# Optimization experiments

Measured on AMD Instinct MI355X. Metric: run time of the kernel, lower is better.

The kernel has to match this reference:

```python
import jax, jax.numpy as jnp
import numpy as np

HIDDEN = 768
N_HEADS = 12
D_HEAD = 64
B, T = 4, 2048


def setup_inputs() -> dict:
    key = jax.random.key(0)
    ks = jax.random.split(key, 5)
    s = 0.02
    return {
        "x": jax.random.normal(ks[0], (B, T, HIDDEN), dtype=jnp.float32),
        "w_q": jax.random.normal(ks[1], (HIDDEN, HIDDEN), dtype=jnp.float32) * s,
        "w_k": jax.random.normal(ks[2], (HIDDEN, HIDDEN), dtype=jnp.float32) * s,
        "w_v": jax.random.normal(ks[3], (HIDDEN, HIDDEN), dtype=jnp.float32) * s,
        "w_o": jax.random.normal(ks[4], (HIDDEN, HIDDEN), dtype=jnp.float32) * s,
    }


def reference(x, w_q, w_k, w_v, w_o):
    # nn.Linear applies x @ W^T; weights here are [out, in] like torch.
    b, t, h = x.shape
    q = (x @ w_q.T).reshape(b, t, N_HEADS, D_HEAD)
    k = (x @ w_k.T).reshape(b, t, N_HEADS, D_HEAD)
    v = (x @ w_v.T).reshape(b, t, N_HEADS, D_HEAD)
    # scores: [b, heads, t, t]
    scores = jnp.einsum("bqhd,bkhd->bhqk", q, k) / jnp.sqrt(jnp.float32(D_HEAD))
    weights = jax.nn.softmax(scores, axis=-1)
    # dropout p=0.0 -> identity
    ctx = jnp.einsum("bhqk,bkhd->bqhd", weights, v).reshape(b, t, h)
    return ctx @ w_o.T
```

## Files before the change

kernel.cpp:

```cpp
#include <hip/hip_runtime.h>

#define HIDDEN 768
#define NH 12
#define DH 64
#define BB 4
#define TT 2048
#define MTOT (BB * TT)

typedef __bf16 bf16x8 __attribute__((ext_vector_type(8)));
typedef short s16x8 __attribute__((ext_vector_type(8)));
typedef float f32x4 __attribute__((ext_vector_type(4)));

__device__ __forceinline__ unsigned short f2b(float f) {
    unsigned u = __builtin_bit_cast(unsigned, f);
    u += 0x7fffu + ((u >> 16) & 1u);
    return (unsigned short)(u >> 16);
}

__device__ __forceinline__ unsigned pack_bf16(float a, float b) {
    return __builtin_amdgcn_perm(__builtin_bit_cast(unsigned, b),
                                 __builtin_bit_cast(unsigned, a), 0x07060302u);
}

typedef const __attribute__((address_space(1))) unsigned int* gas_ptr;
typedef __attribute__((address_space(3))) unsigned int* las_ptr;
__device__ __forceinline__ void gload16(const void* g, void* l) {
    __builtin_amdgcn_global_load_lds((gas_ptr)(uintptr_t)g, (las_ptr)(uintptr_t)l, 16, 0, 0);
}

__global__ __launch_bounds__(256) void cvt_all(const float* __restrict__ x,
                                               const float* __restrict__ wq,
                                               const float* __restrict__ wk,
                                               const float* __restrict__ wv,
                                               const float* __restrict__ wo,
                                               unsigned short* __restrict__ out) {
    const size_t NX8 = (size_t)MTOT * HIDDEN / 8;
    const size_t NW8 = (size_t)HIDDEN * HIDDEN / 8;
    size_t i = (size_t)blockIdx.x * 256 + threadIdx.x;
    const float* src;
    size_t off = i;
    float scale = 1.0f;
    if (i < NX8) { src = x; }
    else if (i < NX8 + NW8) { src = wq; off = i - NX8; scale = 0.18033688011112042f; }
    else if (i < NX8 + 2 * NW8) { src = wk; off = i - NX8 - NW8; }
    else if (i < NX8 + 3 * NW8) { src = wv; off = i - NX8 - 2 * NW8; }
    else { src = wo; off = i - NX8 - 3 * NW8; }
    const float4* p = (const float4*)src + off * 2;
    float4 a = p[0], b = p[1];
    union { uint4 u; unsigned short s[8]; } t;
    t.s[0] = f2b(a.x * scale); t.s[1] = f2b(a.y * scale);
    t.s[2] = f2b(a.z * scale); t.s[3] = f2b(a.w * scale);
    t.s[4] = f2b(b.x * scale); t.s[5] = f2b(b.y * scale);
    t.s[6] = f2b(b.z * scale); t.s[7] = f2b(b.w * scale);
    ((uint4*)out)[i] = t.u;
}

template <int MODE, int MROWS>
__device__ __forceinline__ void gemm_body(const unsigned short* __restrict__ A,
                                          const unsigned short* __restrict__ Bm,
                                          float* __restrict__ Cf,
                                          unsigned short* __restrict__ Cb,
                                          int mBase, int nBase, int N) {
    __shared__ __align__(16) unsigned short Al[MROWS][64];
    __shared__ __align__(16) unsigned short Bl[128][64];
    const int MT = MROWS / 32;
    const int tid = threadIdx.x;
    const int lane = tid & 63;
    const int wave = tid >> 6;
    const int quad = lane >> 4;
    const int l16 = lane & 15;
    const int mw = (wave >> 1) * (MROWS / 2);
    const int nw = (wave & 1) * 64;
    const int r8 = lane >> 3;
    const int swiz = ((lane & 7) ^ r8) * 8;
    const unsigned short* Asrc = A + (size_t)(mBase + wave * (MROWS / 4) + r8) * HIDDEN + swiz;
    const unsigned short* Bsrc = Bm + (size_t)(nBase + wave * 32 + r8) * HIDDEN + swiz;

    f32x4 acc[MT][4];
#pragma unroll
    for (int mt = 0; mt < MT; ++mt)
#pragma unroll
        for (int nt = 0; nt < 4; ++nt) acc[mt][nt] = (f32x4){0.f, 0.f, 0.f, 0.f};

    for (int kb = 0; kb < HIDDEN / 64; ++kb) {
        if (kb) __syncthreads();
#pragma unroll
        for (int i = 0; i < MROWS / 32; ++i)
            gload16(Asrc + (size_t)i * 8 * HIDDEN + kb * 64,
                    &Al[wave * (MROWS / 4) + i * 8][0]);
#pragma unroll
        for (int j = 0; j < 4; ++j)
            gload16(Bsrc + (size_t)j * 8 * HIDDEN + kb * 64, &Bl[wave * 32 + j * 8][0]);
        __syncthreads();
#pragma unroll
        for (int ks = 0; ks < 2; ++ks) {
            const int cc = ((ks * 4 + quad) ^ (l16 & 7)) * 8;
            bf16x8 af[MT], bf[4];
#pragma unroll
            for (int mt = 0; mt < MT; ++mt)
                af[mt] = *(const bf16x8*)&Al[mw + mt * 16 + l16][cc];
#pragma unroll
            for (int nt = 0; nt < 4; ++nt)
                bf[nt] = *(const bf16x8*)&Bl[nw + nt * 16 + l16][cc];
#pragma unroll
            for (int mt = 0; mt < MT; ++mt)
#pragma unroll
                for (int nt = 0; nt < 4; ++nt)
                    acc[mt][nt] = __builtin_amdgcn_mfma_f32_16x16x32_bf16(
                        af[mt], bf[nt], acc[mt][nt], 0, 0, 0);
        }
    }

#pragma unroll
    for (int mt = 0; mt < MT; ++mt)
#pragma unroll
        for (int nt = 0; nt < 4; ++nt) {
            if (MODE == 2) {
                ushort4 h;
                h.x = f2b(acc[mt][nt][0]); h.y = f2b(acc[mt][nt][1]);
                h.z = f2b(acc[mt][nt][2]); h.w = f2b(acc[mt][nt][3]);
                int m0 = mBase + mw + mt * 16 + quad * 4;
                int col = nBase + nw + nt * 16 + l16;
                *(ushort4*)&Cb[(size_t)col * MTOT + m0] = h;
            } else {
#pragma unroll
                for (int r = 0; r < 4; ++r) {
                    int row = mBase + mw + mt * 16 + quad * 4 + r;
                    int col = nBase + nw + nt * 16 + l16;
                    float v = acc[mt][nt][r];
                    if (MODE == 1)
                        Cf[(size_t)row * N + col] = v;
                    else
                        Cb[(size_t)row * N + col] = f2b(v);
                }
            }
        }
}

__global__ __launch_bounds__(256, 2) void gemm_qkv(const unsigned short* __restrict__ A,
                                                   const unsigned short* __restrict__ W0,
                                                   unsigned short* __restrict__ C0,
                                                   unsigned short* __restrict__ VT) {
    __shared__ __align__(16) unsigned short Al[64][64];
    __shared__ __align__(16) unsigned short Bl[3][128][64];
    const size_t NWW = (size_t)HIDDEN * HIDDEN;
    const size_t NX = (size_t)MTOT * HIDDEN;
    const int tid = threadIdx.x;
    const int lane = tid & 63;
    const int wave = tid >> 6;
    const int quad = lane >> 4;
    const int l16 = lane & 15;
    const int rx = l16 & 7;
    const int mw = (wave >> 1) * 32;
    const int nw = (wave & 1) * 64;
    const int r8 = lane >> 3;
    const int swiz = ((lane & 7) ^ r8) * 8;
    const int mBase = blockIdx.x * 64;
    const int nBase = blockIdx.y * 128;
    const unsigned short* Asrc = A + (size_t)(mBase + wave * 16 + r8) * HIDDEN + swiz;
    const unsigned short* Bsrc = W0 + (size_t)(nBase + wave * 32 + r8) * HIDDEN + swiz;

    f32x4 acc[3][2][4];
#pragma unroll
    for (int w = 0; w < 3; ++w)
#pragma unroll
        for (int mt = 0; mt < 2; ++mt)
#pragma unroll
            for (int nt = 0; nt < 4; ++nt) acc[w][mt][nt] = (f32x4){0.f, 0.f, 0.f, 0.f};

    for (int kb = 0; kb < HIDDEN / 64; ++kb) {
        if (kb) __syncthreads();
#pragma unroll
        for (int i = 0; i < 2; ++i)
            gload16(Asrc + (size_t)i * 8 * HIDDEN + kb * 64, &Al[wave * 16 + i * 8][0]);
#pragma unroll
        for (int w = 0; w < 3; ++w)
#pragma unroll
            for (int j = 0; j < 4; ++j)
                gload16(Bsrc + (size_t)w * NWW + (size_t)j * 8 * HIDDEN + kb * 64,
                        &Bl[w][wave * 32 + j * 8][0]);
        __syncthreads();
#pragma unroll
        for (int ks = 0; ks < 2; ++ks) {
            const int cc = ((ks * 4 + quad) ^ rx) * 8;
            bf16x8 af[2];
#pragma unroll
            for (int mt = 0; mt < 2; ++mt)
                af[mt] = *(const bf16x8*)&Al[mw + mt * 16 + l16][cc];
#pragma unroll
            for (int w = 0; w < 3; ++w) {
                bf16x8 bf[4];
#pragma unroll
                for (int nt = 0; nt < 4; ++nt)
                    bf[nt] = *(const bf16x8*)&Bl[w][nw + nt * 16 + l16][cc];
                __builtin_amdgcn_s_setprio(1);
#pragma unroll
                for (int mt = 0; mt < 2; ++mt)
#pragma unroll
                    for (int nt = 0; nt < 4; ++nt)
                        acc[w][mt][nt] = __builtin_amdgcn_mfma_f32_16x16x32_bf16(
                            af[mt], bf[nt], acc[w][mt][nt], 0, 0, 0);
                __builtin_amdgcn_s_setprio(0);
            }
        }
    }

#pragma unroll
    for (int w = 0; w < 3; ++w)
#pragma unroll
        for (int mt = 0; mt < 2; ++mt)
#pragma unroll
            for (int nt = 0; nt < 4; ++nt) {
                if (w == 2) {
                    ushort4 h;
                    h.x = f2b(acc[2][mt][nt][0]); h.y = f2b(acc[2][mt][nt][1]);
                    h.z = f2b(acc[2][mt][nt][2]); h.w = f2b(acc[2][mt][nt][3]);
                    int m0 = mBase + mw + mt * 16 + quad * 4;
                    int col = nBase + nw + nt * 16 + l16;
                    *(ushort4*)&VT[(size_t)col * MTOT + m0] = h;
                } else {
                    unsigned short* Cb = C0 + (size_t)w * NX;
#pragma unroll
                    for (int r = 0; r < 4; ++r) {
                        int row = mBase + mw + mt * 16 + quad * 4 + r;
                        int col = nBase + nw + nt * 16 + l16;
                        Cb[(size_t)row * HIDDEN + col] = f2b(acc[w][mt][nt][r]);
                    }
                }
            }
}

__global__ __launch_bounds__(256, 4) void gemm_out(const unsigned short* __restrict__ A,
                                                   const unsigned short* __restrict__ Bm,
                                                   float* __restrict__ Cf) {
    gemm_body<1, 128>(A, Bm, Cf, nullptr, blockIdx.x * 128, blockIdx.y * 128, HIDDEN);
}

__global__ __launch_bounds__(256, 3) void attn_kernel(const unsigned short* __restrict__ Qg,
                                                      const unsigned short* __restrict__ Kg,
                                                      const unsigned short* __restrict__ VTg,
                                                      unsigned short* __restrict__ Ctx) {
    __shared__ __align__(16) unsigned short Kl[2][64][64];
    __shared__ __align__(16) unsigned short Vl[2][64][64];
    __shared__ __align__(16) unsigned int Pl[4][32][32];
    const int tid = threadIdx.x;
    const int lane = tid & 63;
    const int wave = tid >> 6;
    const int quad = lane >> 4;
    const int l16 = lane & 15;
    const int qt = blockIdx.y;
    const int bh = blockIdx.x;
    const int b = bh / NH, h = bh % NH;
    const int qrow0 = b * TT + qt * 128;
    const int col0 = h * DH;

    const int srow = wave * 16 + (lane >> 3);
    const int swiz = ((lane & 7) ^ (lane >> 3)) * 8;
    const unsigned short* Ksrc = Kg + (size_t)(b * TT + srow) * HIDDEN + col0 + swiz;
    const unsigned short* Vsrc = VTg + (size_t)(col0 + srow) * MTOT + b * TT + swiz;

    auto stage = [&](int buf, int kt) {
#pragma unroll
        for (int i = 0; i < 2; ++i) {
            gload16(Ksrc + (size_t)(kt * 64 + i * 8) * HIDDEN, &Kl[buf][wave * 16 + i * 8][0]);
            gload16(Vsrc + (size_t)(i * 8) * MTOT + kt * 64, &Vl[buf][wave * 16 + i * 8][0]);
        }
    };

    bf16x8 qf[2][2];
#pragma unroll
    for (int mt = 0; mt < 2; ++mt)
#pragma unroll
        for (int ks = 0; ks < 2; ++ks)
            qf[mt][ks] = *(const bf16x8*)&Qg[(size_t)(qrow0 + wave * 32 + mt * 16 + l16) * HIDDEN +
                                             col0 + ks * 32 + quad * 8];

    s16x8 osv;
#pragma unroll
    for (int e = 0; e < 8; ++e) osv[e] = 0x3F80;
    const bf16x8 ones = __builtin_bit_cast(bf16x8, osv);

    f32x4 o[2][4];
    f32x4 lacc[2];
#pragma unroll
    for (int mt = 0; mt < 2; ++mt) {
        lacc[mt] = (f32x4){0.f, 0.f, 0.f, 0.f};
#pragma unroll
        for (int nt = 0; nt < 4; ++nt) o[mt][nt] = (f32x4){0.f, 0.f, 0.f, 0.f};
    }

    const int rx = l16 & 7;
    const f32x4 z4 = (f32x4){0.f, 0.f, 0.f, 0.f};

    stage(0, 0);
    for (int kt = 0; kt < TT / 64; ++kt) {
        __syncthreads();
        if (kt + 1 < TT / 64) stage((kt + 1) & 1, kt + 1);
        const int buf = kt & 1;

        f32x4 s[2][4];
#pragma unroll
        for (int ks = 0; ks < 2; ++ks) {
            const int cc = ((ks * 4 + quad) ^ rx) * 8;
            bf16x8 kf[4];
#pragma unroll
            for (int nt = 0; nt < 4; ++nt)
                kf[nt] = *(const bf16x8*)&Kl[buf][nt * 16 + l16][cc];
            __builtin_amdgcn_s_setprio(1);
#pragma unroll
            for (int mt = 0; mt < 2; ++mt)
#pragma unroll
                for (int nt = 0; nt < 4; ++nt)
                    s[mt][nt] = __builtin_amdgcn_mfma_f32_16x16x32_bf16(
                        kf[nt], qf[mt][ks], ks ? s[mt][nt] : z4, 0, 0, 0);
            __builtin_amdgcn_s_setprio(0);
        }

#pragma unroll
        for (int mt = 0; mt < 2; ++mt) {
            const int row = mt * 16 + l16;
#pragma unroll
            for (int nt = 0; nt < 4; ++nt) {
                float p0 = __builtin_amdgcn_exp2f(s[mt][nt][0]);
                float p1 = __builtin_amdgcn_exp2f(s[mt][nt][1]);
                float p2 = __builtin_amdgcn_exp2f(s[mt][nt][2]);
                float p3 = __builtin_amdgcn_exp2f(s[mt][nt][3]);
                uint2 w;
                w.x = pack_bf16(p0, p1);
                w.y = pack_bf16(p2, p3);
                const int unit = 2 * nt + (quad >> 1);
                *(uint2*)&Pl[wave][row][(((unit ^ rx) << 2) | ((quad & 1) << 1))] = w;
            }
        }

#pragma unroll
        for (int ks = 0; ks < 2; ++ks) {
            const int cc = ((ks * 4 + quad) ^ rx) * 8;
            bf16x8 pf[2], vf[4];
#pragma unroll
            for (int mt = 0; mt < 2; ++mt)
                pf[mt] = *(const bf16x8*)((const char*)&Pl[wave][mt * 16 + l16][0] +
                                          ((((ks * 4 + quad) ^ rx) << 4)));
#pragma unroll
            for (int nt = 0; nt < 4; ++nt)
                vf[nt] = *(const bf16x8*)&Vl[buf][nt * 16 + l16][cc];
            __builtin_amdgcn_s_setprio(1);
#pragma unroll
            for (int mt = 0; mt < 2; ++mt)
                lacc[mt] = __builtin_amdgcn_mfma_f32_16x16x32_bf16(pf[mt], ones, lacc[mt], 0, 0, 0);
#pragma unroll
            for (int mt = 0; mt < 2; ++mt)
#pragma unroll
                for (int nt = 0; nt < 4; ++nt)
                    o[mt][nt] = __builtin_amdgcn_mfma_f32_16x16x32_bf16(pf[mt], vf[nt],
                                                                        o[mt][nt], 0, 0, 0);
            __builtin_amdgcn_s_setprio(0);
        }
    }

#pragma unroll
    for (int mt = 0; mt < 2; ++mt)
#pragma unroll
        for (int r = 0; r < 4; ++r) {
            float inv = __builtin_amdgcn_rcpf(lacc[mt][r]);
            int row = qrow0 + wave * 32 + mt * 16 + quad * 4 + r;
#pragma unroll
            for (int nt = 0; nt < 4; ++nt)
                Ctx[(size_t)row * HIDDEN + col0 + nt * 16 + l16] = f2b(o[mt][nt][r] * inv);
        }
}

extern "C" void kernel_launch(void* const* d_in, const int* in_sizes, int n_in,
                              void* d_out, int out_size, void* d_ws, size_t ws_size,
                              hipStream_t stream) {
    const float* x = (const float*)d_in[0];
    const float* wq = (const float*)d_in[1];
    const float* wk = (const float*)d_in[2];
    const float* wv = (const float*)d_in[3];
    const float* wo = (const float*)d_in[4];
    float* out = (float*)d_out;

    const size_t NX = (size_t)MTOT * HIDDEN;
    const size_t NW = (size_t)HIDDEN * HIDDEN;
    unsigned short* ws = (unsigned short*)d_ws;
    unsigned short* xb = ws;
    unsigned short* wqb = xb + NX;
    unsigned short* wob = wqb + 3 * NW;
    unsigned short* qb = wob + NW;
    unsigned short* kb = qb + NX;
    unsigned short* cb = kb + NX;
    unsigned short* vtb = cb + NX;

    cvt_all<<<(int)((NX + 4 * NW) / 8 / 256), 256, 0, stream>>>(x, wq, wk, wv, wo, xb);

    gemm_qkv<<<dim3(MTOT / 64, 6), 256, 0, stream>>>(xb, wqb, qb, vtb);

    attn_kernel<<<dim3(BB * NH, TT / 128), 256, 0, stream>>>(qb, kb, vtb, cb);

    gemm_out<<<dim3(MTOT / 128, 6), 256, 0, stream>>>(cb, wob, out);
}
```

Baseline: 198.9 us.

## Fuse fp32-to-bf16 conversion of x into the QKV GEMM A-tile load

The standalone conversion kernel now handles only the weights. The QKV GEMM reads x in fp32 directly, converts it to bf16 in registers and writes it to LDS, replacing the async global-to-LDS copy. This drops a full write and re-read of the bf16 copy of x. In exchange x is read 6 times in fp32 (once per N block), the A load becomes synchronous through registers, and the unused MODE 2 transposed-store path in gemm_body is removed.

```diff
diff --git a/kernel.cpp b/kernel.cpp
--- a/kernel.cpp
+++ b/kernel.cpp
@@ -22,29 +22,34 @@
                                  __builtin_bit_cast(unsigned, a), 0x07060302u);
 }
 
+__device__ __forceinline__ unsigned rne_u(float f) {
+    unsigned u = __builtin_bit_cast(unsigned, f);
+    return u + 0x7fffu + ((u >> 16) & 1u);
+}
+__device__ __forceinline__ unsigned pack2_rne(float a, float b) {
+    return __builtin_amdgcn_perm(rne_u(b), rne_u(a), 0x07060302u);
+}
+
 typedef const __attribute__((address_space(1))) unsigned int* gas_ptr;
 typedef __attribute__((address_space(3))) unsigned int* las_ptr;
 __device__ __forceinline__ void gload16(const void* g, void* l) {
     __builtin_amdgcn_global_load_lds((gas_ptr)(uintptr_t)g, (las_ptr)(uintptr_t)l, 16, 0, 0);
 }
 
-__global__ __launch_bounds__(256) void cvt_all(const float* __restrict__ x,
-                                               const float* __restrict__ wq,
+__global__ __launch_bounds__(256) void cvt_all(const float* __restrict__ wq,
                                                const float* __restrict__ wk,
                                                const float* __restrict__ wv,
                                                const float* __restrict__ wo,
                                                unsigned short* __restrict__ out) {
-    const size_t NX8 = (size_t)MTOT * HIDDEN / 8;
     const size_t NW8 = (size_t)HIDDEN * HIDDEN / 8;
     size_t i = (size_t)blockIdx.x * 256 + threadIdx.x;
     const float* src;
     size_t off = i;
     float scale = 1.0f;
-    if (i < NX8) { src = x; }
-    else if (i < NX8 + NW8) { src = wq; off = i - NX8; scale = 0.18033688011112042f; }
-    else if (i < NX8 + 2 * NW8) { src = wk; off = i - NX8 - NW8; }
-    else if (i < NX8 + 3 * NW8) { src = wv; off = i - NX8 - 2 * NW8; }
-    else { src = wo; off = i - NX8 - 3 * NW8; }
+    if (i < NW8) { src = wq; scale = 0.18033688011112042f; }
+    else if (i < 2 * NW8) { src = wk; off = i - NW8; }
+    else if (i < 3 * NW8) { src = wv; off = i - 2 * NW8; }
+    else { src = wo; off = i - 3 * NW8; }
     const float4* p = (const float4*)src + off * 2;
     float4 a = p[0], b = p[1];
     union { uint4 u; unsigned short s[8]; } t;
@@ -115,29 +120,20 @@
     for (int mt = 0; mt < MT; ++mt)
 #pragma unroll
         for (int nt = 0; nt < 4; ++nt) {
-            if (MODE == 2) {
-                ushort4 h;
-                h.x = f2b(acc[mt][nt][0]); h.y = f2b(acc[mt][nt][1]);
-                h.z = f2b(acc[mt][nt][2]); h.w = f2b(acc[mt][nt][3]);
-                int m0 = mBase + mw + mt * 16 + quad * 4;
+#pragma unroll
+            for (int r = 0; r < 4; ++r) {
+                int row = mBase + mw + mt * 16 + quad * 4 + r;
                 int col = nBase + nw + nt * 16 + l16;
-                *(ushort4*)&Cb[(size_t)col * MTOT + m0] = h;
-            } else {
-#pragma unroll
-                for (int r = 0; r < 4; ++r) {
-                    int row = mBase + mw + mt * 16 + quad * 4 + r;
-                    int col = nBase + nw + nt * 16 + l16;
-                    float v = acc[mt][nt][r];
-                    if (MODE == 1)
-                        Cf[(size_t)row * N + col] = v;
-                    else
-                        Cb[(size_t)row * N + col] = f2b(v);
-                }
+                float v = acc[mt][nt][r];
+                if (MODE == 1)
+                    Cf[(size_t)row * N + col] = v;
+                else
+                    Cb[(size_t)row * N + col] = f2b(v);
             }
         }
 }
 
-__global__ __launch_bounds__(256, 2) void gemm_qkv(const unsigned short* __restrict__ A,
+__global__ __launch_bounds__(256, 2) void gemm_qkv(const float* __restrict__ X,
                                                    const unsigned short* __restrict__ W0,
                                                    unsigned short* __restrict__ C0,
                                                    unsigned short* __restrict__ VT) {
@@ -157,7 +153,7 @@
     const int swiz = ((lane & 7) ^ r8) * 8;
     const int mBase = blockIdx.x * 64;
     const int nBase = blockIdx.y * 128;
-    const unsigned short* Asrc = A + (size_t)(mBase + wave * 16 + r8) * HIDDEN + swiz;
+    const float* Axsrc = X + (size_t)(mBase + wave * 16 + r8) * HIDDEN + swiz;
     const unsigned short* Bsrc = W0 + (size_t)(nBase + wave * 32 + r8) * HIDDEN + swiz;
 
     f32x4 acc[3][2][4];
@@ -170,15 +166,23 @@
 
     for (int kb = 0; kb < HIDDEN / 64; ++kb) {
         if (kb) __syncthreads();
-#pragma unroll
-        for (int i = 0; i < 2; ++i)
-            gload16(Asrc + (size_t)i * 8 * HIDDEN + kb * 64, &Al[wave * 16 + i * 8][0]);
 #pragma unroll
         for (int w = 0; w < 3; ++w)
 #pragma unroll
             for (int j = 0; j < 4; ++j)
                 gload16(Bsrc + (size_t)w * NWW + (size_t)j * 8 * HIDDEN + kb * 64,
                         &Bl[w][wave * 32 + j * 8][0]);
+#pragma unroll
+        for (int i = 0; i < 2; ++i) {
+            const float4* p = (const float4*)(Axsrc + (size_t)i * 8 * HIDDEN + kb * 64);
+            float4 a = p[0], b = p[1];
+            uint4 wv4;
+            wv4.x = pack2_rne(a.x, a.y);
+            wv4.y = pack2_rne(a.z, a.w);
+            wv4.z = pack2_rne(b.x, b.y);
+            wv4.w = pack2_rne(b.z, b.w);
+            *(uint4*)((char*)&Al[wave * 16 + i * 8][0] + lane * 16) = wv4;
+        }
         __syncthreads();
 #pragma unroll
         for (int ks = 0; ks < 2; ++ks) {
@@ -383,17 +387,16 @@
     const size_t NX = (size_t)MTOT * HIDDEN;
     const size_t NW = (size_t)HIDDEN * HIDDEN;
     unsigned short* ws = (unsigned short*)d_ws;
-    unsigned short* xb = ws;
-    unsigned short* wqb = xb + NX;
+    unsigned short* wqb = ws;
     unsigned short* wob = wqb + 3 * NW;
     unsigned short* qb = wob + NW;
     unsigned short* kb = qb + NX;
     unsigned short* cb = kb + NX;
     unsigned short* vtb = cb + NX;
 
-    cvt_all<<<(int)((NX + 4 * NW) / 8 / 256), 256, 0, stream>>>(x, wq, wk, wv, wo, xb);
-
-    gemm_qkv<<<dim3(MTOT / 64, 6), 256, 0, stream>>>(xb, wqb, qb, vtb);
+    cvt_all<<<(int)(4 * NW / 8 / 256), 256, 0, stream>>>(wq, wk, wv, wo, wqb);
+
+    gemm_qkv<<<dim3(MTOT / 64, 6), 256, 0, stream>>>(x, wqb, qb, vtb);
 
     attn_kernel<<<dim3(BB * NH, TT / 128), 256, 0, stream>>>(qb, kb, vtb, cb);
 
```

After: 203.6 us. 2.3% more time.
